# Kernel tuning notes

Hardware: AMD Instinct MI355X
Metric: run time of the kernel (lower is better)

## Reference

```python
import jax, jax.numpy as jnp
import numpy as np

EPS = 1e-6


def setup_inputs() -> dict:
    key = jax.random.key(0)
    k1, k2, k3 = jax.random.split(key, 3)
    B, H, L, D = 1, 16, 1024, 64
    return {
        "q": jax.random.normal(k1, (B, H, L, D), dtype=jnp.float32),
        "k": jax.random.normal(k2, (B, H, L, D), dtype=jnp.float32),
        "v": jax.random.normal(k3, (B, H, L, D), dtype=jnp.float32),
    }


def reference(q, k, v):
    bsz, head_num, tgt_len, dim = q.shape
    src_len = k.shape[2]
    m = max(src_len, tgt_len)

    # flatten batch*heads: [N, L, D]
    q = jax.nn.relu(q.reshape(-1, tgt_len, dim))
    k = jax.nn.relu(k.reshape(-1, src_len, dim))
    v = v.reshape(-1, src_len, dim)

    # cosFormer re-weighting index: pi/2 * (1..m) / m, shape [1, m, 1]
    idx = (np.pi / 2) * jnp.arange(1, m + 1, dtype=q.dtype).reshape(1, -1, 1) / m
    sin_w = jnp.sin(idx)
    cos_w = jnp.cos(idx)

    # feature-mapped q/k: [N, L, 2D]
    q_ = jnp.concatenate([q * sin_w[:, :tgt_len, :], q * cos_w[:, :tgt_len, :]], axis=-1)
    k_ = jnp.concatenate([k * sin_w[:, :src_len, :], k * cos_w[:, :src_len, :]], axis=-1)

    # causal linear attention via cumulative outer products
    kv_ = jnp.einsum("nld,nlm->nldm", k_, v)          # [N, L, 2D, D]
    kv_cum = jnp.cumsum(kv_, axis=1)
    qkv = jnp.einsum("nld,nldm->nlm", q_, kv_cum)      # [N, L, D]

    k_cum = jnp.cumsum(k_, axis=1)                      # [N, L, 2D]
    denom = jnp.clip(jnp.einsum("nld,nld->nl", q_, k_cum), EPS, None)

    out = qkv / denom[..., None]
    return out.reshape(bsz, head_num, tgt_len, dim)
```

## Files before the change

### kernel.cpp

```cpp
#include <hip/hip_runtime.h>

namespace {
constexpr int Hh = 16;
constexpr int Ll = 1024;
constexpr int Dd = 64;
constexpr int Cc = 64;
constexpr int NCHUNK = Ll / Cc;
constexpr float PI_HALF = 1.5707963267948966f;
constexpr float EPSV = 1e-6f;
constexpr int S1 = 72;
constexpr int SA = 200;
constexpr int SB = 136;
constexpr int SV = 200;
}

typedef __attribute__((ext_vector_type(8))) short short8;
typedef __attribute__((ext_vector_type(4))) float floatx4;

__device__ __forceinline__ unsigned short f2bf(float x) {
    unsigned int u = __float_as_uint(x);
    unsigned int r = u + 0x7fffu + ((u >> 16) & 1u);
    return (unsigned short)(r >> 16);
}

__device__ __forceinline__ int sw1(int row, int j) {
    return (j & 7) | ((((j >> 3) ^ (row >> 3)) & 7) << 3);
}

__global__ __launch_bounds__(256)
void cf_fused(const float* __restrict__ qin, const float* __restrict__ kin,
              const float* __restrict__ vin, float* __restrict__ out) {
    const int c = blockIdx.x, h = blockIdx.y;
    const int tid = threadIdx.x;
    __shared__ unsigned short Ak[128 * S1];
    __shared__ unsigned short Bv1[80 * S1];
    __shared__ unsigned short Aq[64 * SA];
    __shared__ unsigned short Bk[80 * SB];
    __shared__ unsigned short Bv[64 * SV];

    const int wave = tid >> 6, lane = tid & 63;
    const int lrow = lane & 15, quad = lane >> 4;

    const size_t hbase = (size_t)h * Ll * Dd;
    const size_t gbase = hbase + (size_t)c * Cc * Dd;

    const float4* q4 = (const float4*)(qin + gbase);
    const float4* k4 = (const float4*)(kin + gbase);
    const float4* v4 = (const float4*)(vin + gbase);
    float4 oq[4], ok[4], ov[4], pk[4], pv[4];
    #pragma unroll
    for (int i = 0; i < 4; ++i) {
        oq[i] = q4[i * 256 + tid];
        ok[i] = k4[i * 256 + tid];
        ov[i] = v4[i * 256 + tid];
    }
    if (c > 0) {
        const float4* kp = (const float4*)(kin + hbase);
        const float4* vp = (const float4*)(vin + hbase);
        #pragma unroll
        for (int i = 0; i < 4; ++i) {
            pk[i] = kp[i * 256 + tid];
            pv[i] = vp[i * 256 + tid];
        }
    }

    #pragma unroll
    for (int i = 0; i < 4; ++i) {
        int e4 = i * 256 + tid;
        int j = e4 >> 4, d4 = (e4 & 15) * 4;
        float th = PI_HALF * (float)(c * Cc + j + 1) * (1.0f / (float)Ll);
        float sj, cj;
        __sincosf(th, &sj, &cj);
        float q0 = fmaxf(oq[i].x, 0.f), q1 = fmaxf(oq[i].y, 0.f);
        float q2 = fmaxf(oq[i].z, 0.f), q3 = fmaxf(oq[i].w, 0.f);
        *(ushort4*)&Aq[j * SA + 64 + d4] =
            make_ushort4(f2bf(q0 * sj), f2bf(q1 * sj), f2bf(q2 * sj), f2bf(q3 * sj));
        *(ushort4*)&Aq[j * SA + 128 + d4] =
            make_ushort4(f2bf(q0 * cj), f2bf(q1 * cj), f2bf(q2 * cj), f2bf(q3 * cj));
        float k0 = fmaxf(ok[i].x, 0.f), k1 = fmaxf(ok[i].y, 0.f);
        float k2 = fmaxf(ok[i].z, 0.f), k3 = fmaxf(ok[i].w, 0.f);
        *(ushort4*)&Bk[j * SB + d4] =
            make_ushort4(f2bf(k0 * sj), f2bf(k1 * sj), f2bf(k2 * sj), f2bf(k3 * sj));
        *(ushort4*)&Bk[j * SB + 64 + d4] =
            make_ushort4(f2bf(k0 * cj), f2bf(k1 * cj), f2bf(k2 * cj), f2bf(k3 * cj));
        Bv[(d4 + 0) * SV + j] = f2bf(ov[i].x);
        Bv[(d4 + 1) * SV + j] = f2bf(ov[i].y);
        Bv[(d4 + 2) * SV + j] = f2bf(ov[i].z);
        Bv[(d4 + 3) * SV + j] = f2bf(ov[i].w);
    }
    #pragma unroll
    for (int i = 0; i < 4; ++i) {
        int z = i * 256 + tid;
        if (z < (15 * SB) / 2) ((unsigned int*)Bk)[(65 * SB) / 2 + z] = 0u;
    }
    if (tid < 64) Bv1[64 * S1 + tid] = 0x3F80;
    if (tid >= 64 && tid < S1) Bv1[64 * S1 + tid] = 0;
    #pragma unroll
    for (int i = 0; i < 3; ++i) {
        int z = i * 256 + tid;
        if (z < (15 * S1) / 2) ((unsigned int*)Bv1)[(65 * S1) / 2 + z] = 0u;
    }

    floatx4 acc[2][5];
    #pragma unroll
    for (int t = 0; t < 2; ++t)
        #pragma unroll
        for (int nt = 0; nt < 5; ++nt)
            acc[t][nt] = (floatx4){0.f, 0.f, 0.f, 0.f};

    for (int cp = 0; cp < c; ++cp) {
        #pragma unroll
        for (int i = 0; i < 4; ++i) {
            int e4 = i * 256 + tid;
            int j = e4 >> 4, d4 = (e4 & 15) * 4;
            float th = PI_HALF * (float)(cp * Cc + j + 1) * (1.0f / (float)Ll);
            float sj, cj;
            __sincosf(th, &sj, &cj);
            float r0 = fmaxf(pk[i].x, 0.f), r1 = fmaxf(pk[i].y, 0.f);
            float r2 = fmaxf(pk[i].z, 0.f), r3 = fmaxf(pk[i].w, 0.f);
            int col = sw1(d4, j);
            Ak[(d4 + 0) * S1 + col] = f2bf(r0 * sj);
            Ak[(d4 + 1) * S1 + col] = f2bf(r1 * sj);
            Ak[(d4 + 2) * S1 + col] = f2bf(r2 * sj);
            Ak[(d4 + 3) * S1 + col] = f2bf(r3 * sj);
            Ak[(64 + d4 + 0) * S1 + col] = f2bf(r0 * cj);
            Ak[(64 + d4 + 1) * S1 + col] = f2bf(r1 * cj);
            Ak[(64 + d4 + 2) * S1 + col] = f2bf(r2 * cj);
            Ak[(64 + d4 + 3) * S1 + col] = f2bf(r3 * cj);
            Bv1[(d4 + 0) * S1 + col] = f2bf(pv[i].x);
            Bv1[(d4 + 1) * S1 + col] = f2bf(pv[i].y);
            Bv1[(d4 + 2) * S1 + col] = f2bf(pv[i].z);
            Bv1[(d4 + 3) * S1 + col] = f2bf(pv[i].w);
        }
        __syncthreads();
        if (cp + 1 < c) {
            const float4* kp = (const float4*)(kin + hbase + (size_t)(cp + 1) * Cc * Dd);
            const float4* vp = (const float4*)(vin + hbase + (size_t)(cp + 1) * Cc * Dd);
            #pragma unroll
            for (int i = 0; i < 4; ++i) {
                pk[i] = kp[i * 256 + tid];
                pv[i] = vp[i * 256 + tid];
            }
        }
        #pragma unroll
        for (int t = 0; t < 2; ++t) {
            int fr = (wave * 2 + t) * 16 + lrow;
            int keyA = (fr >> 3) & 7;
            short8 a0 = *(const short8*)&Ak[fr * S1 + ((quad ^ keyA) << 3)];
            short8 a1 = *(const short8*)&Ak[fr * S1 + (((4 + quad) ^ keyA) << 3)];
            #pragma unroll
            for (int nt = 0; nt < 5; ++nt) {
                int nr = nt * 16 + lrow;
                int keyB = (nr >> 3) & 7;
                short8 b0 = *(const short8*)&Bv1[nr * S1 + ((quad ^ keyB) << 3)];
                short8 b1 = *(const short8*)&Bv1[nr * S1 + (((4 + quad) ^ keyB) << 3)];
                acc[t][nt] = __builtin_amdgcn_mfma_f32_16x16x32_bf16(a0, b0, acc[t][nt], 0, 0, 0);
                acc[t][nt] = __builtin_amdgcn_mfma_f32_16x16x32_bf16(a1, b1, acc[t][nt], 0, 0, 0);
            }
        }
        __syncthreads();
    }

    #pragma unroll
    for (int t = 0; t < 2; ++t) {
        int fb = wave * 32 + t * 16 + quad * 4;
        #pragma unroll
        for (int nt = 0; nt < 4; ++nt) {
            int d = nt * 16 + lrow;
            *(ushort4*)&Bv[d * SV + 64 + fb] =
                make_ushort4(f2bf(acc[t][nt][0]), f2bf(acc[t][nt][1]),
                             f2bf(acc[t][nt][2]), f2bf(acc[t][nt][3]));
        }
        if (lrow == 0)
            *(ushort4*)&Bk[64 * SB + fb] =
                make_ushort4(f2bf(acc[t][4][0]), f2bf(acc[t][4][1]),
                             f2bf(acc[t][4][2]), f2bf(acc[t][4][3]));
    }
    __syncthreads();

    const int l0 = wave * 16;
    const int arow = (l0 + lrow) * SA;
    short8 a1f[4];
    #pragma unroll
    for (int ks = 0; ks < 4; ++ks)
        a1f[ks] = *(const short8*)&Aq[arow + 64 + ks * 32 + quad * 8];
    floatx4 rs = {0.f, 0.f, 0.f, 0.f};
    #pragma unroll
    for (int nt = 0; nt < 5; ++nt) {
        floatx4 s = {0.f, 0.f, 0.f, 0.f};
        #pragma unroll
        for (int ks = 0; ks < 4; ++ks) {
            short8 bf = *(const short8*)&Bk[(nt * 16 + lrow) * SB + ks * 32 + quad * 8];
            s = __builtin_amdgcn_mfma_f32_16x16x32_bf16(a1f[ks], bf, s, 0, 0, 0);
        }
        if (nt < 4) {
            int j = nt * 16 + lrow;
            #pragma unroll
            for (int r = 0; r < 4; ++r) {
                int l = l0 + quad * 4 + r;
                float m = (j <= l) ? s[r] : 0.f;
                s[r] = m;
                Aq[l * SA + j] = f2bf(m);
            }
        }
        rs += s;
    }
    #pragma unroll
    for (int m = 1; m <= 8; m <<= 1) {
        rs[0] += __shfl_xor(rs[0], m);
        rs[1] += __shfl_xor(rs[1], m);
        rs[2] += __shfl_xor(rs[2], m);
        rs[3] += __shfl_xor(rs[3], m);
    }
    float inv[4];
    #pragma unroll
    for (int r = 0; r < 4; ++r) inv[r] = 1.0f / fmaxf(rs[r], EPSV);

    __syncthreads();

    short8 s0 = *(const short8*)&Aq[arow + quad * 8];
    short8 s1 = *(const short8*)&Aq[arow + 32 + quad * 8];
    #pragma unroll
    for (int nt = 0; nt < 4; ++nt) {
        const int brow = (nt * 16 + lrow) * SV;
        floatx4 a2 = {0.f, 0.f, 0.f, 0.f};
        a2 = __builtin_amdgcn_mfma_f32_16x16x32_bf16(
                 s0, *(const short8*)&Bv[brow + quad * 8], a2, 0, 0, 0);
        a2 = __builtin_amdgcn_mfma_f32_16x16x32_bf16(
                 s1, *(const short8*)&Bv[brow + 32 + quad * 8], a2, 0, 0, 0);
        #pragma unroll
        for (int ks = 2; ks < 6; ++ks) {
            short8 bf = *(const short8*)&Bv[brow + ks * 32 + quad * 8];
            a2 = __builtin_amdgcn_mfma_f32_16x16x32_bf16(a1f[ks - 2], bf, a2, 0, 0, 0);
        }
        #pragma unroll
        for (int r = 0; r < 4; ++r) {
            int l = l0 + quad * 4 + r;
            out[gbase + (size_t)l * Dd + nt * 16 + lrow] = a2[r] * inv[r];
        }
    }
}

extern "C" void kernel_launch(void* const* d_in, const int* in_sizes, int n_in,
                              void* d_out, int out_size, void* d_ws, size_t ws_size,
                              hipStream_t stream) {
    const float* q = (const float*)d_in[0];
    const float* k = (const float*)d_in[1];
    const float* v = (const float*)d_in[2];
    float* out = (float*)d_out;
    (void)d_ws; (void)ws_size;
    cf_fused<<<dim3(NCHUNK, Hh), 256, 0, stream>>>(q, k, v, out);
}
```

Baseline: 87.19 us.

## Compute per-chunk KV states once and share via grid barrier and prefix sum

Each block used to recompute the KV outer products for every earlier chunk of its head, so later chunks did up to 15 times the MFMA work. Now each block computes only its own chunk state, writes it as bf16 to workspace, waits at a global atomic barrier, then sums the earlier chunk states from memory. This removes the quadratic redundant compute but adds a grid-wide spin barrier that assumes all 256 blocks are co-resident, plus a memset and global traffic. Summing bf16-rounded states adds rounding error compared with accumulating in fp32.

```diff
diff --git a/kernel.cpp b/kernel.cpp
--- a/kernel.cpp
+++ b/kernel.cpp
@@ -6,12 +6,14 @@
 constexpr int Dd = 64;
 constexpr int Cc = 64;
 constexpr int NCHUNK = Ll / Cc;
+constexpr int NBLK = Hh * NCHUNK;
 constexpr float PI_HALF = 1.5707963267948966f;
 constexpr float EPSV = 1e-6f;
 constexpr int S1 = 72;
 constexpr int SA = 200;
 constexpr int SB = 136;
 constexpr int SV = 200;
+constexpr int STATE_E = 128 * 64;
 }
 
 typedef __attribute__((ext_vector_type(8))) short short8;
@@ -22,14 +24,23 @@
     unsigned int r = u + 0x7fffu + ((u >> 16) & 1u);
     return (unsigned short)(r >> 16);
 }
+__device__ __forceinline__ float bfhi(unsigned int u) {
+    return __uint_as_float(u & 0xffff0000u);
+}
+__device__ __forceinline__ float bflo(unsigned int u) {
+    return __uint_as_float(u << 16);
+}
 
 __device__ __forceinline__ int sw1(int row, int j) {
     return (j & 7) | ((((j >> 3) ^ (row >> 3)) & 7) << 3);
 }
 
 __global__ __launch_bounds__(256)
-void cf_fused(const float* __restrict__ qin, const float* __restrict__ kin,
-              const float* __restrict__ vin, float* __restrict__ out) {
+void cf_onekernel(const float* __restrict__ qin, const float* __restrict__ kin,
+                  const float* __restrict__ vin, float* __restrict__ out,
+                  unsigned int* __restrict__ bar,
+                  unsigned short* __restrict__ wskv,
+                  unsigned short* __restrict__ wsks) {
     const int c = blockIdx.x, h = blockIdx.y;
     const int tid = threadIdx.x;
     __shared__ unsigned short Ak[128 * S1];
@@ -41,28 +52,10 @@
     const int wave = tid >> 6, lane = tid & 63;
     const int lrow = lane & 15, quad = lane >> 4;
 
-    const size_t hbase = (size_t)h * Ll * Dd;
-    const size_t gbase = hbase + (size_t)c * Cc * Dd;
-
+    const size_t gbase = ((size_t)h * Ll + (size_t)c * Cc) * Dd;
     const float4* q4 = (const float4*)(qin + gbase);
     const float4* k4 = (const float4*)(kin + gbase);
     const float4* v4 = (const float4*)(vin + gbase);
-    float4 oq[4], ok[4], ov[4], pk[4], pv[4];
-    #pragma unroll
-    for (int i = 0; i < 4; ++i) {
-        oq[i] = q4[i * 256 + tid];
-        ok[i] = k4[i * 256 + tid];
-        ov[i] = v4[i * 256 + tid];
-    }
-    if (c > 0) {
-        const float4* kp = (const float4*)(kin + hbase);
-        const float4* vp = (const float4*)(vin + hbase);
-        #pragma unroll
-        for (int i = 0; i < 4; ++i) {
-            pk[i] = kp[i * 256 + tid];
-            pv[i] = vp[i * 256 + tid];
-        }
-    }
 
     #pragma unroll
     for (int i = 0; i < 4; ++i) {
@@ -71,35 +64,56 @@
         float th = PI_HALF * (float)(c * Cc + j + 1) * (1.0f / (float)Ll);
         float sj, cj;
         __sincosf(th, &sj, &cj);
-        float q0 = fmaxf(oq[i].x, 0.f), q1 = fmaxf(oq[i].y, 0.f);
-        float q2 = fmaxf(oq[i].z, 0.f), q3 = fmaxf(oq[i].w, 0.f);
+        float4 qv = q4[e4];
+        float q0 = fmaxf(qv.x, 0.f), q1 = fmaxf(qv.y, 0.f);
+        float q2 = fmaxf(qv.z, 0.f), q3 = fmaxf(qv.w, 0.f);
         *(ushort4*)&Aq[j * SA + 64 + d4] =
             make_ushort4(f2bf(q0 * sj), f2bf(q1 * sj), f2bf(q2 * sj), f2bf(q3 * sj));
         *(ushort4*)&Aq[j * SA + 128 + d4] =
             make_ushort4(f2bf(q0 * cj), f2bf(q1 * cj), f2bf(q2 * cj), f2bf(q3 * cj));
-        float k0 = fmaxf(ok[i].x, 0.f), k1 = fmaxf(ok[i].y, 0.f);
-        float k2 = fmaxf(ok[i].z, 0.f), k3 = fmaxf(ok[i].w, 0.f);
-        *(ushort4*)&Bk[j * SB + d4] =
-            make_ushort4(f2bf(k0 * sj), f2bf(k1 * sj), f2bf(k2 * sj), f2bf(k3 * sj));
-        *(ushort4*)&Bk[j * SB + 64 + d4] =
-            make_ushort4(f2bf(k0 * cj), f2bf(k1 * cj), f2bf(k2 * cj), f2bf(k3 * cj));
-        Bv[(d4 + 0) * SV + j] = f2bf(ov[i].x);
-        Bv[(d4 + 1) * SV + j] = f2bf(ov[i].y);
-        Bv[(d4 + 2) * SV + j] = f2bf(ov[i].z);
-        Bv[(d4 + 3) * SV + j] = f2bf(ov[i].w);
+        float4 kx = k4[e4];
+        float k0 = fmaxf(kx.x, 0.f), k1 = fmaxf(kx.y, 0.f);
+        float k2 = fmaxf(kx.z, 0.f), k3 = fmaxf(kx.w, 0.f);
+        unsigned short ks0 = f2bf(k0 * sj), ks1 = f2bf(k1 * sj);
+        unsigned short ks2 = f2bf(k2 * sj), ks3 = f2bf(k3 * sj);
+        unsigned short kc0 = f2bf(k0 * cj), kc1 = f2bf(k1 * cj);
+        unsigned short kc2 = f2bf(k2 * cj), kc3 = f2bf(k3 * cj);
+        *(ushort4*)&Bk[j * SB + d4] = make_ushort4(ks0, ks1, ks2, ks3);
+        *(ushort4*)&Bk[j * SB + 64 + d4] = make_ushort4(kc0, kc1, kc2, kc3);
+        int col = sw1(d4, j);
+        Ak[(d4 + 0) * S1 + col] = ks0;
+        Ak[(d4 + 1) * S1 + col] = ks1;
+        Ak[(d4 + 2) * S1 + col] = ks2;
+        Ak[(d4 + 3) * S1 + col] = ks3;
+        Ak[(64 + d4 + 0) * S1 + col] = kc0;
+        Ak[(64 + d4 + 1) * S1 + col] = kc1;
+        Ak[(64 + d4 + 2) * S1 + col] = kc2;
+        Ak[(64 + d4 + 3) * S1 + col] = kc3;
+        float4 vx = v4[e4];
+        unsigned short v0 = f2bf(vx.x), v1 = f2bf(vx.y);
+        unsigned short v2 = f2bf(vx.z), v3 = f2bf(vx.w);
+        Bv[(d4 + 0) * SV + j] = v0;
+        Bv[(d4 + 1) * SV + j] = v1;
+        Bv[(d4 + 2) * SV + j] = v2;
+        Bv[(d4 + 3) * SV + j] = v3;
+        Bv1[(d4 + 0) * S1 + col] = v0;
+        Bv1[(d4 + 1) * S1 + col] = v1;
+        Bv1[(d4 + 2) * S1 + col] = v2;
+        Bv1[(d4 + 3) * S1 + col] = v3;
+    }
+    if (tid < 64) Bv1[64 * S1 + tid] = 0x3F80;
+    if (tid >= 64 && tid < S1) Bv1[64 * S1 + tid] = 0;
+    #pragma unroll
+    for (int i = 0; i < 3; ++i) {
+        int z = i * 256 + tid;
+        if (z < (15 * S1) / 2) ((unsigned int*)Bv1)[(65 * S1) / 2 + z] = 0u;
     }
     #pragma unroll
     for (int i = 0; i < 4; ++i) {
         int z = i * 256 + tid;
         if (z < (15 * SB) / 2) ((unsigned int*)Bk)[(65 * SB) / 2 + z] = 0u;
     }
-    if (tid < 64) Bv1[64 * S1 + tid] = 0x3F80;
-    if (tid >= 64 && tid < S1) Bv1[64 * S1 + tid] = 0;
-    #pragma unroll
-    for (int i = 0; i < 3; ++i) {
-        int z = i * 256 + tid;
-        if (z < (15 * S1) / 2) ((unsigned int*)Bv1)[(65 * S1) / 2 + z] = 0u;
-    }
+    __syncthreads();
 
     floatx4 acc[2][5];
     #pragma unroll
@@ -107,74 +121,89 @@
         #pragma unroll
         for (int nt = 0; nt < 5; ++nt)
             acc[t][nt] = (floatx4){0.f, 0.f, 0.f, 0.f};
-
-    for (int cp = 0; cp < c; ++cp) {
+    #pragma unroll
+    for (int t = 0; t < 2; ++t) {
+        int fr = (wave * 2 + t) * 16 + lrow;
+        int keyA = (fr >> 3) & 7;
+        short8 a0 = *(const short8*)&Ak[fr * S1 + ((quad ^ keyA) << 3)];
+        short8 a1 = *(const short8*)&Ak[fr * S1 + (((4 + quad) ^ keyA) << 3)];
+        #pragma unroll
+        for (int nt = 0; nt < 5; ++nt) {
+            int nr = nt * 16 + lrow;
+            int keyB = (nr >> 3) & 7;
+            short8 b0 = *(const short8*)&Bv1[nr * S1 + ((quad ^ keyB) << 3)];
+            short8 b1 = *(const short8*)&Bv1[nr * S1 + (((4 + quad) ^ keyB) << 3)];
+            acc[t][nt] = __builtin_amdgcn_mfma_f32_16x16x32_bf16(a0, b0, acc[t][nt], 0, 0, 0);
+            acc[t][nt] = __builtin_amdgcn_mfma_f32_16x16x32_bf16(a1, b1, acc[t][nt], 0, 0, 0);
+        }
+    }
+    {
+        unsigned short* st = wskv + (size_t)(h * NCHUNK + c) * STATE_E;
+        #pragma unroll
+        for (int t = 0; t < 2; ++t) {
+            int fb = (wave * 2 + t) * 16 + quad * 4;
+            #pragma unroll
+            for (int nt = 0; nt < 4; ++nt) {
+                int d = nt * 16 + lrow;
+                *(ushort4*)(st + d * 128 + fb) =
+                    make_ushort4(f2bf(acc[t][nt][0]), f2bf(acc[t][nt][1]),
+                                 f2bf(acc[t][nt][2]), f2bf(acc[t][nt][3]));
+            }
+            if (lrow == 0)
+                *(ushort4*)(wsks + (size_t)(h * NCHUNK + c) * 128 + fb) =
+                    make_ushort4(f2bf(acc[t][4][0]), f2bf(acc[t][4][1]),
+                                 f2bf(acc[t][4][2]), f2bf(acc[t][4][3]));
+        }
+    }
+
+    __syncthreads();
+    if (tid == 0) {
+        __threadfence();
+        __hip_atomic_fetch_add(bar, 1u, __ATOMIC_ACQ_REL, __HIP_MEMORY_SCOPE_AGENT);
+        while (__hip_atomic_load(bar, __ATOMIC_ACQUIRE, __HIP_MEMORY_SCOPE_AGENT)
+               < (unsigned)NBLK)
+            __builtin_amdgcn_s_sleep(8);
+    }
+    __syncthreads();
+
+    {
+        const unsigned short* base = wskv + (size_t)h * NCHUNK * STATE_E;
         #pragma unroll
         for (int i = 0; i < 4; ++i) {
-            int e4 = i * 256 + tid;
-            int j = e4 >> 4, d4 = (e4 & 15) * 4;
-            float th = PI_HALF * (float)(cp * Cc + j + 1) * (1.0f / (float)Ll);
-            float sj, cj;
-            __sincosf(th, &sj, &cj);
-            float r0 = fmaxf(pk[i].x, 0.f), r1 = fmaxf(pk[i].y, 0.f);
-            float r2 = fmaxf(pk[i].z, 0.f), r3 = fmaxf(pk[i].w, 0.f);
-            int col = sw1(d4, j);
-            Ak[(d4 + 0) * S1 + col] = f2bf(r0 * sj);
-            Ak[(d4 + 1) * S1 + col] = f2bf(r1 * sj);
-            Ak[(d4 + 2) * S1 + col] = f2bf(r2 * sj);
-            Ak[(d4 + 3) * S1 + col] = f2bf(r3 * sj);
-            Ak[(64 + d4 + 0) * S1 + col] = f2bf(r0 * cj);
-            Ak[(64 + d4 + 1) * S1 + col] = f2bf(r1 * cj);
-            Ak[(64 + d4 + 2) * S1 + col] = f2bf(r2 * cj);
-            Ak[(64 + d4 + 3) * S1 + col] = f2bf(r3 * cj);
-            Bv1[(d4 + 0) * S1 + col] = f2bf(pv[i].x);
-            Bv1[(d4 + 1) * S1 + col] = f2bf(pv[i].y);
-            Bv1[(d4 + 2) * S1 + col] = f2bf(pv[i].z);
-            Bv1[(d4 + 3) * S1 + col] = f2bf(pv[i].w);
-        }
-        __syncthreads();
-        if (cp + 1 < c) {
-            const float4* kp = (const float4*)(kin + hbase + (size_t)(cp + 1) * Cc * Dd);
-            const float4* vp = (const float4*)(vin + hbase + (size_t)(cp + 1) * Cc * Dd);
-            #pragma unroll
-            for (int i = 0; i < 4; ++i) {
-                pk[i] = kp[i * 256 + tid];
-                pv[i] = vp[i * 256 + tid];
-            }
-        }
-        #pragma unroll
-        for (int t = 0; t < 2; ++t) {
-            int fr = (wave * 2 + t) * 16 + lrow;
-            int keyA = (fr >> 3) & 7;
-            short8 a0 = *(const short8*)&Ak[fr * S1 + ((quad ^ keyA) << 3)];
-            short8 a1 = *(const short8*)&Ak[fr * S1 + (((4 + quad) ^ keyA) << 3)];
-            #pragma unroll
-            for (int nt = 0; nt < 5; ++nt) {
-                int nr = nt * 16 + lrow;
-                int keyB = (nr >> 3) & 7;
-                short8 b0 = *(const short8*)&Bv1[nr * S1 + ((quad ^ keyB) << 3)];
-                short8 b1 = *(const short8*)&Bv1[nr * S1 + (((4 + quad) ^ keyB) << 3)];
-                acc[t][nt] = __builtin_amdgcn_mfma_f32_16x16x32_bf16(a0, b0, acc[t][nt], 0, 0, 0);
-                acc[t][nt] = __builtin_amdgcn_mfma_f32_16x16x32_bf16(a1, b1, acc[t][nt], 0, 0, 0);
-            }
-        }
-        __syncthreads();
-    }
-
-    #pragma unroll
-    for (int t = 0; t < 2; ++t) {
-        int fb = wave * 32 + t * 16 + quad * 4;
-        #pragma unroll
-        for (int nt = 0; nt < 4; ++nt) {
-            int d = nt * 16 + lrow;
-            *(ushort4*)&Bv[d * SV + 64 + fb] =
-                make_ushort4(f2bf(acc[t][nt][0]), f2bf(acc[t][nt][1]),
-                             f2bf(acc[t][nt][2]), f2bf(acc[t][nt][3]));
-        }
-        if (lrow == 0)
-            *(ushort4*)&Bk[64 * SB + fb] =
-                make_ushort4(f2bf(acc[t][4][0]), f2bf(acc[t][4][1]),
-                             f2bf(acc[t][4][2]), f2bf(acc[t][4][3]));
+            int idx = i * 256 + tid;
+            int d = idx >> 4, f8 = (idx & 15) * 8;
+            float s[8];
+            #pragma unroll
+            for (int x = 0; x < 8; ++x) s[x] = 0.f;
+            for (int cp = 0; cp < c; ++cp) {
+                uint4 u = *(const uint4*)(base + (size_t)cp * STATE_E + d * 128 + f8);
+                s[0] += bflo(u.x); s[1] += bfhi(u.x);
+                s[2] += bflo(u.y); s[3] += bfhi(u.y);
+                s[4] += bflo(u.z); s[5] += bfhi(u.z);
+                s[6] += bflo(u.w); s[7] += bfhi(u.w);
+            }
+            *(ushort4*)&Bv[d * SV + 64 + f8] =
+                make_ushort4(f2bf(s[0]), f2bf(s[1]), f2bf(s[2]), f2bf(s[3]));
+            *(ushort4*)&Bv[d * SV + 64 + f8 + 4] =
+                make_ushort4(f2bf(s[4]), f2bf(s[5]), f2bf(s[6]), f2bf(s[7]));
+        }
+        if (tid < 16) {
+            const unsigned short* kb = wsks + (size_t)h * NCHUNK * 128;
+            float s[8];
+            #pragma unroll
+            for (int x = 0; x < 8; ++x) s[x] = 0.f;
+            for (int cp = 0; cp < c; ++cp) {
+                uint4 u = *(const uint4*)(kb + cp * 128 + tid * 8);
+                s[0] += bflo(u.x); s[1] += bfhi(u.x);
+                s[2] += bflo(u.y); s[3] += bfhi(u.y);
+                s[4] += bflo(u.z); s[5] += bfhi(u.z);
+                s[6] += bflo(u.w); s[7] += bfhi(u.w);
+            }
+            *(ushort4*)&Bk[64 * SB + tid * 8] =
+                make_ushort4(f2bf(s[0]), f2bf(s[1]), f2bf(s[2]), f2bf(s[3]));
+            *(ushort4*)&Bk[64 * SB + tid * 8 + 4] =
+                make_ushort4(f2bf(s[4]), f2bf(s[5]), f2bf(s[6]), f2bf(s[7]));
+        }
     }
     __syncthreads();
 
@@ -248,6 +277,9 @@
     const float* k = (const float*)d_in[1];
     const float* v = (const float*)d_in[2];
     float* out = (float*)d_out;
-    (void)d_ws; (void)ws_size;
-    cf_fused<<<dim3(NCHUNK, Hh), 256, 0, stream>>>(q, k, v, out);
-}
+    unsigned int* bar = (unsigned int*)d_ws;
+    unsigned short* wskv = (unsigned short*)d_ws + 128;
+    unsigned short* wsks = wskv + (size_t)NBLK * STATE_E;
+    hipMemsetAsync(bar, 0, 64, stream);
+    cf_onekernel<<<dim3(NCHUNK, Hh), 256, 0, stream>>>(q, k, v, out, bar, wskv, wsks);
+}
```

Result: slower. 116.1 us (+33.2%).
